# Kernel optimization log

Measured on AMD Instinct MI355X. Metric: run time of the kernel, lower is better.

The kernel has to match this reference:

```python
import jax, jax.numpy as jnp
import numpy as np

N_NODES = 100_000
N_EDGES = 800_000
D = 96
BN_EPS = 1e-5
LEAKY_SLOPE = 0.01


def setup_inputs() -> dict:
    key = jax.random.key(0)
    ks = jax.random.split(key, 9)
    x = jax.random.normal(ks[0], (N_NODES, D), dtype=jnp.float32)
    edge_index = jax.random.randint(ks[1], (2, N_EDGES), 0, N_NODES, dtype=jnp.int64)
    s = 0.05
    return {
        "x": x,
        "edge_index": edge_index,
        # SAGEConv #1 (mean aggregator, bias=False)
        "W_self1": jax.random.normal(ks[2], (D, D), dtype=jnp.float32) * s,
        "W_neigh1": jax.random.normal(ks[3], (D, D), dtype=jnp.float32) * s,
        # SAGEConv #2 (pool aggregator): fc_pool has bias, fc_self/fc_neigh bias=False
        "W_pool": jax.random.normal(ks[4], (D, D), dtype=jnp.float32) * s,
        "b_pool": jax.random.normal(ks[5], (D,), dtype=jnp.float32) * s,
        "W_self2": jax.random.normal(ks[6], (D, D), dtype=jnp.float32) * s,
        "W_neigh2": jax.random.normal(ks[7], (D, D), dtype=jnp.float32) * s,
        # BatchNorm affine params
        "g1": jnp.ones((D,), jnp.float32),
        "beta1": jnp.zeros((D,), jnp.float32),
        "g2": jnp.ones((D,), jnp.float32),
        "beta2": jnp.zeros((D,), jnp.float32),
    }


def _batch_norm(h, gamma, beta):
    # training-mode BatchNorm1d: biased batch stats over nodes
    mu = h.mean(axis=0)
    var = jnp.mean(jnp.square(h - mu), axis=0)
    return gamma * (h - mu) * jax.lax.rsqrt(var + BN_EPS) + beta


def _forward(x, edge_index, W_self1, W_neigh1, W_pool, b_pool, W_self2, W_neigh2,
             g1, beta1, g2, beta2):
    src, dst = edge_index[0], edge_index[1]
    n = x.shape[0]
    deg = jax.ops.segment_sum(jnp.ones((src.shape[0],), x.dtype), dst, num_segments=n)

    # ---- SAGEConv (mean): h_neigh = mean_{u in N(v)} x_u ; out = x W_self + h_neigh W_neigh
    agg_sum = jax.ops.segment_sum(x[src], dst, num_segments=n)          # [N, D]
    h_mean = agg_sum / jnp.maximum(deg, 1.0)[:, None]                   # 0 for isolated nodes
    out1 = x @ W_self1 + h_mean @ W_neigh1
    out1 = _batch_norm(out1, g1, beta1)

    # ---- SAGEConv (pool): h_neigh = max_{u in N(v)} relu(x_u W_pool + b_pool)
    hp = jax.nn.relu(x @ W_pool + b_pool)                               # [N, D]
    agg_max = jax.ops.segment_max(hp[src], dst, num_segments=n)        # -inf where empty
    h_max = jnp.where(deg[:, None] > 0, agg_max, 0.0)
    out2 = x @ W_self2 + h_max @ W_neigh2
    out2 = _batch_norm(out2, g2, beta2)

    return jax.nn.leaky_relu(out1 + out2, negative_slope=LEAKY_SLOPE)


def reference(x, edge_index, W_self1, W_neigh1, W_pool, b_pool, W_self2, W_neigh2,
              g1, beta1, g2, beta2):
    return _forward(x, edge_index, W_self1, W_neigh1, W_pool, b_pool,
                    W_self2, W_neigh2, g1, beta1, g2, beta2)
```

## Files before the change

### kernel.cpp

```cpp
#include <hip/hip_runtime.h>

#define NN 100000
#define NE 800000
#define DD 96
#define NROWPAD 100096
#define GBLK 782
#define SCAN_BLOCKS 100
#define SCAN_CHUNK 1000

typedef __attribute__((ext_vector_type(8))) short bf16x8;
typedef __attribute__((ext_vector_type(4))) float f32x4;
typedef unsigned short u16;
typedef unsigned int u32;

#define MFMA16 __builtin_amdgcn_mfma_f32_16x16x32_bf16

#define OFF_DEG      0u
#define OFF_ROWSTART 100000u
#define OFF_CURSOR   200004u
#define OFF_BSUM     300004u
#define OFF_STATS    300132u
#define OFF_PARAMS   300516u
#define OFF_WT       300900u
#define OFF_CSR      323940u
#define OFF_XH       1123940u
#define OFF_HMBF     10733156u
#define OFF_HXBF     15537764u

__device__ __forceinline__ u16 f2b(float f) {
  u32 u = __float_as_uint(f);
  u += 0x7FFFu + ((u >> 16) & 1u);
  return (u16)(u >> 16);
}
__device__ __forceinline__ float b2f(short h) {
  return __uint_as_float(((u32)(u16)h) << 16);
}

__global__ void wprep_kernel(const float* __restrict__ Ws1, const float* __restrict__ Wn1,
                             const float* __restrict__ Ws2, const float* __restrict__ Wn2,
                             const float* __restrict__ Wp, u16* __restrict__ wt) {
  int idx = blockIdx.x * 256 + threadIdx.x;
  if (idx >= 5 * 9216) return;
  int m = idx / 9216, r = idx % 9216;
  int k = r / 96, c = r % 96;
  const float* W = (m == 0) ? Ws1 : (m == 1) ? Wn1 : (m == 2) ? Ws2 : (m == 3) ? Wn2 : Wp;
  wt[m * 9216 + c * 96 + k] = f2b(W[k * 96 + c]);
}

__global__ void deg_kernel(const int* __restrict__ dst, int* __restrict__ deg) {
  int e = blockIdx.x * blockDim.x + threadIdx.x;
  if (e >= NE) return;
  atomicAdd(&deg[dst[e]], 1);
}

__global__ void scan_sum_kernel(const int* __restrict__ deg, int* __restrict__ bsum) {
  __shared__ int red[256];
  int t = threadIdx.x;
  int base = blockIdx.x * SCAN_CHUNK;
  int s = 0;
  for (int i = t; i < SCAN_CHUNK; i += 256) s += deg[base + i];
  red[t] = s;
  __syncthreads();
  for (int off = 128; off > 0; off >>= 1) {
    if (t < off) red[t] += red[t + off];
    __syncthreads();
  }
  if (t == 0) bsum[blockIdx.x] = red[0];
}

__global__ void scan_bsum_kernel(int* __restrict__ bsum, int* __restrict__ row_start) {
  __shared__ int sm[128];
  int t = threadIdx.x;
  int v = (t < SCAN_BLOCKS) ? bsum[t] : 0;
  sm[t] = v;
  __syncthreads();
  for (int off = 1; off < 128; off <<= 1) {
    int u = 0;
    if (t >= off) u = sm[t - off];
    __syncthreads();
    if (t >= off) sm[t] += u;
    __syncthreads();
  }
  if (t < SCAN_BLOCKS) bsum[t] = sm[t] - v;
  if (t == SCAN_BLOCKS - 1) row_start[NN] = sm[t];
}

__global__ void scan_final_kernel(const int* __restrict__ deg,
                                  const int* __restrict__ bsum,
                                  int* __restrict__ row_start,
                                  int* __restrict__ cursor) {
  __shared__ int sm[256];
  int t = threadIdx.x;
  int base = blockIdx.x * SCAN_CHUNK + t * 4;
  int4 d = {0, 0, 0, 0};
  if (t < 250) d = *reinterpret_cast<const int4*>(deg + base);
  int tot = d.x + d.y + d.z + d.w;
  sm[t] = tot;
  __syncthreads();
  for (int off = 1; off < 256; off <<= 1) {
    int u = 0;
    if (t >= off) u = sm[t - off];
    __syncthreads();
    if (t >= off) sm[t] += u;
    __syncthreads();
  }
  if (t < 250) {
    int run = bsum[blockIdx.x] + sm[t] - tot;
    int4 rs;
    rs.x = run;
    rs.y = run + d.x;
    rs.z = run + d.x + d.y;
    rs.w = run + d.x + d.y + d.z;
    *reinterpret_cast<int4*>(row_start + base) = rs;
    *reinterpret_cast<int4*>(cursor + base) = rs;
  }
}

__global__ void fill_csr_kernel(const int* __restrict__ src,
                                const int* __restrict__ dst,
                                int* __restrict__ cursor,
                                int* __restrict__ csr) {
  int e = blockIdx.x * blockDim.x + threadIdx.x;
  if (e >= NE) return;
  int pos = atomicAdd(&cursor[dst[e]], 1);
  csr[pos] = src[e];
}

__global__ __launch_bounds__(512) void hp_gemm_kernel(const float* __restrict__ x,
                                                      const u16* __restrict__ wt,
                                                      const float* __restrict__ bp,
                                                      u16* __restrict__ xh) {
  __shared__ bf16x8 wl[1152];
  int t = threadIdx.x;
  const bf16x8* wg = reinterpret_cast<const bf16x8*>(wt + 4 * 9216);
  for (int j = t; j < 1152; j += 512) wl[j] = wg[j];
  __syncthreads();
  int w = t >> 6, lane = t & 63;
  int i = lane & 15, g = lane >> 4;
  int row_base = blockIdx.x * 128 + w * 16;
  int grow_a = row_base + i;
  int lrow = grow_a < NN ? grow_a : NN - 1;
  const float4* xr = reinterpret_cast<const float4*>(x + (size_t)lrow * 96);
  bf16x8* xhv = reinterpret_cast<bf16x8*>(xh);
  bf16x8 ax[3];
#pragma unroll
  for (int kb = 0; kb < 3; ++kb) {
    float4 p = xr[(kb * 4 + g) * 2];
    float4 q = xr[(kb * 4 + g) * 2 + 1];
    bf16x8 v;
    v[0] = (short)f2b(p.x); v[1] = (short)f2b(p.y); v[2] = (short)f2b(p.z); v[3] = (short)f2b(p.w);
    v[4] = (short)f2b(q.x); v[5] = (short)f2b(q.y); v[6] = (short)f2b(q.z); v[7] = (short)f2b(q.w);
    ax[kb] = v;
    xhv[(size_t)grow_a * 24 + kb * 4 + g] = v;
  }
  for (int nt = 0; nt < 6; ++nt) {
    f32x4 acc = {0.f, 0.f, 0.f, 0.f};
    int bch = (nt * 16 + i) * 12;
#pragma unroll
    for (int kb = 0; kb < 3; ++kb)
      acc = MFMA16(ax[kb], wl[bch + kb * 4 + g], acc, 0, 0, 0);
    int col = nt * 16 + i;
    float bias = bp[col];
#pragma unroll
    for (int r = 0; r < 4; ++r) {
      int grow = row_base + g * 4 + r;
      xh[(size_t)grow * 192 + 96 + col] = f2b(fmaxf(acc[r] + bias, 0.0f));
    }
  }
}

__global__ __launch_bounds__(256) void gather_kernel(const u16* __restrict__ xh,
                                                     const int* __restrict__ row_start,
                                                     const int* __restrict__ csr,
                                                     u16* __restrict__ hmbf,
                                                     u16* __restrict__ hxbf) {
  int t = threadIdx.x;
  int node = blockIdx.x * 32 + (t & 31);
  int slot = t >> 5;
  bool isMax = slot >= 4;
  if (node >= NN) return;
  int beg = row_start[node], end = row_start[node + 1];
  int cbase = slot * 3;
  const bf16x8* XH = reinterpret_cast<const bf16x8*>(xh);
  float acc0[8], acc1[8], acc2[8];
#pragma unroll
  for (int j = 0; j < 8; ++j) { acc0[j] = 0.f; acc1[j] = 0.f; acc2[j] = 0.f; }
  int e = beg;
  for (; e + 2 <= end; e += 2) {
    size_t b0 = (size_t)csr[e] * 24 + cbase;
    size_t b1 = (size_t)csr[e + 1] * 24 + cbase;
    bf16x8 a0 = XH[b0], a1 = XH[b0 + 1], a2 = XH[b0 + 2];
    bf16x8 c0 = XH[b1], c1 = XH[b1 + 1], c2 = XH[b1 + 2];
    if (isMax) {
#pragma unroll
      for (int j = 0; j < 8; ++j) {
        acc0[j] = fmaxf(acc0[j], fmaxf(b2f(a0[j]), b2f(c0[j])));
        acc1[j] = fmaxf(acc1[j], fmaxf(b2f(a1[j]), b2f(c1[j])));
        acc2[j] = fmaxf(acc2[j], fmaxf(b2f(a2[j]), b2f(c2[j])));
      }
    } else {
#pragma unroll
      for (int j = 0; j < 8; ++j) {
        acc0[j] += b2f(a0[j]) + b2f(c0[j]);
        acc1[j] += b2f(a1[j]) + b2f(c1[j]);
        acc2[j] += b2f(a2[j]) + b2f(c2[j]);
      }
    }
  }
  if (e < end) {
    size_t b0 = (size_t)csr[e] * 24 + cbase;
    bf16x8 a0 = XH[b0], a1 = XH[b0 + 1], a2 = XH[b0 + 2];
    if (isMax) {
#pragma unroll
      for (int j = 0; j < 8; ++j) {
        acc0[j] = fmaxf(acc0[j], b2f(a0[j]));
        acc1[j] = fmaxf(acc1[j], b2f(a1[j]));
        acc2[j] = fmaxf(acc2[j], b2f(a2[j]));
      }
    } else {
#pragma unroll
      for (int j = 0; j < 8; ++j) {
        acc0[j] += b2f(a0[j]);
        acc1[j] += b2f(a1[j]);
        acc2[j] += b2f(a2[j]);
      }
    }
  }
  float scl = isMax ? 1.0f : ((end > beg) ? 1.0f / (float)(end - beg) : 0.0f);
  bf16x8 v0, v1, v2;
#pragma unroll
  for (int j = 0; j < 8; ++j) {
    v0[j] = (short)f2b(acc0[j] * scl);
    v1[j] = (short)f2b(acc1[j] * scl);
    v2[j] = (short)f2b(acc2[j] * scl);
  }
  u16* dstp = isMax ? hxbf : hmbf;
  int ccol = isMax ? (slot - 4) * 3 : slot * 3;
  size_t ob = (size_t)node * 12 + ccol;
  bf16x8* dv = reinterpret_cast<bf16x8*>(dstp);
  dv[ob] = v0; dv[ob + 1] = v1; dv[ob + 2] = v2;
}

__global__ __launch_bounds__(512) void dualgemm_kernel(const u16* __restrict__ xh,
                                                       const u16* __restrict__ hmbf,
                                                       const u16* __restrict__ hxbf,
                                                       const u16* __restrict__ wt,
                                                       float* __restrict__ stats,
                                                       const float* __restrict__ params,
                                                       float* __restrict__ out,
                                                       int mode) {
  __shared__ bf16x8 wl[4608];
  __shared__ float smst[384];
  int t = threadIdx.x;
  const bf16x8* wg = reinterpret_cast<const bf16x8*>(wt);
  for (int j = t; j < 4608; j += 512) wl[j] = wg[j];
  if (mode == 0)
    for (int j = t; j < 384; j += 512) smst[j] = 0.f;
  __syncthreads();
  int w = t >> 6, lane = t & 63;
  int i = lane & 15, g = lane >> 4;
  int row_base = blockIdx.x * 128 + w * 16;
  size_t arowx = (size_t)(row_base + i) * 24;
  size_t arowh = (size_t)(row_base + i) * 12;
  bf16x8 ax[3], am[3], ah[3];
#pragma unroll
  for (int kb = 0; kb < 3; ++kb) {
    ax[kb] = reinterpret_cast<const bf16x8*>(xh)[arowx + kb * 4 + g];
    am[kb] = reinterpret_cast<const bf16x8*>(hmbf)[arowh + kb * 4 + g];
    ah[kb] = reinterpret_cast<const bf16x8*>(hxbf)[arowh + kb * 4 + g];
  }
  for (int nt = 0; nt < 6; ++nt) {
    f32x4 a1 = {0.f, 0.f, 0.f, 0.f}, a2 = {0.f, 0.f, 0.f, 0.f};
    int bch = (nt * 16 + i) * 12;
#pragma unroll
    for (int kb = 0; kb < 3; ++kb) {
      int bc = bch + kb * 4 + g;
      a1 = MFMA16(ax[kb], wl[bc], a1, 0, 0, 0);
      a1 = MFMA16(am[kb], wl[1152 + bc], a1, 0, 0, 0);
      a2 = MFMA16(ax[kb], wl[2304 + bc], a2, 0, 0, 0);
      a2 = MFMA16(ah[kb], wl[3456 + bc], a2, 0, 0, 0);
    }
    int col = nt * 16 + i;
    if (mode == 0) {
      float s1 = 0, q1 = 0, s2 = 0, q2 = 0;
#pragma unroll
      for (int r = 0; r < 4; ++r) {
        int grow = row_base + g * 4 + r;
        if (grow < NN) {
          float v = a1[r], u = a2[r];
          s1 += v; q1 += v * v; s2 += u; q2 += u * u;
        }
      }
      s1 += __shfl_xor(s1, 16); q1 += __shfl_xor(q1, 16);
      s2 += __shfl_xor(s2, 16); q2 += __shfl_xor(q2, 16);
      s1 += __shfl_xor(s1, 32); q1 += __shfl_xor(q1, 32);
      s2 += __shfl_xor(s2, 32); q2 += __shfl_xor(q2, 32);
      if (g == 0) {
        atomicAdd(&smst[col], s1);
        atomicAdd(&smst[96 + col], q1);
        atomicAdd(&smst[192 + col], s2);
        atomicAdd(&smst[288 + col], q2);
      }
    } else {
      float p1 = params[col], c1 = params[96 + col];
      float p2 = params[192 + col], c2 = params[288 + col];
#pragma unroll
      for (int r = 0; r < 4; ++r) {
        int grow = row_base + g * 4 + r;
        if (grow < NN) {
          float v = p1 * a1[r] + c1 + p2 * a2[r] + c2;
          v = v > 0.f ? v : 0.01f * v;
          out[(size_t)grow * 96 + col] = v;
        }
      }
    }
  }
  if (mode == 0) {
    __syncthreads();
    for (int j = t; j < 384; j += 512) atomicAdd(&stats[j], smst[j]);
  }
}

__global__ void finalize_kernel(const float* __restrict__ stats,
                                const float* __restrict__ g1, const float* __restrict__ beta1,
                                const float* __restrict__ g2, const float* __restrict__ beta2,
                                float* __restrict__ params) {
  int c = threadIdx.x;
  if (c >= 96) return;
  const float inv_n = 1.0f / NN;
  float mu1 = stats[c] * inv_n;
  float var1 = fmaxf(stats[96 + c] * inv_n - mu1 * mu1, 0.0f);
  float is1 = rsqrtf(var1 + 1e-5f);
  float a1 = g1[c] * is1;
  params[c] = a1;
  params[96 + c] = beta1[c] - a1 * mu1;
  float mu2 = stats[192 + c] * inv_n;
  float var2 = fmaxf(stats[288 + c] * inv_n - mu2 * mu2, 0.0f);
  float is2 = rsqrtf(var2 + 1e-5f);
  float a2 = g2[c] * is2;
  params[192 + c] = a2;
  params[288 + c] = beta2[c] - a2 * mu2;
}

extern "C" void kernel_launch(void* const* d_in, const int* in_sizes, int n_in,
                              void* d_out, int out_size, void* d_ws, size_t ws_size,
                              hipStream_t stream) {
  const float* x       = (const float*)d_in[0];
  const int*   ei      = (const int*)d_in[1];
  const float* W_self1 = (const float*)d_in[2];
  const float* W_neigh1= (const float*)d_in[3];
  const float* W_pool  = (const float*)d_in[4];
  const float* b_pool  = (const float*)d_in[5];
  const float* W_self2 = (const float*)d_in[6];
  const float* W_neigh2= (const float*)d_in[7];
  const float* g1      = (const float*)d_in[8];
  const float* beta1   = (const float*)d_in[9];
  const float* g2      = (const float*)d_in[10];
  const float* beta2   = (const float*)d_in[11];
  float* out = (float*)d_out;

  float* ws = (float*)d_ws;
  int*   deg       = (int*)(ws + OFF_DEG);
  int*   row_start = (int*)(ws + OFF_ROWSTART);
  int*   cursor    = (int*)(ws + OFF_CURSOR);
  int*   bsum      = (int*)(ws + OFF_BSUM);
  float* stats     = ws + OFF_STATS;
  float* params    = ws + OFF_PARAMS;
  u16*   wt        = (u16*)(ws + OFF_WT);
  int*   csr       = (int*)(ws + OFF_CSR);
  u16*   xh        = (u16*)(ws + OFF_XH);
  u16*   hmbf      = (u16*)(ws + OFF_HMBF);
  u16*   hxbf      = (u16*)(ws + OFF_HXBF);

  const int* src = ei;
  const int* dst = ei + NE;

  hipMemsetAsync(deg, 0, NN * sizeof(int), stream);
  hipMemsetAsync(stats, 0, 384 * sizeof(float), stream);

  wprep_kernel<<<(5 * 9216 + 255) / 256, 256, 0, stream>>>(W_self1, W_neigh1, W_self2,
                                                           W_neigh2, W_pool, wt);

  deg_kernel<<<(NE + 255) / 256, 256, 0, stream>>>(dst, deg);
  scan_sum_kernel<<<SCAN_BLOCKS, 256, 0, stream>>>(deg, bsum);
  scan_bsum_kernel<<<1, 128, 0, stream>>>(bsum, row_start);
  scan_final_kernel<<<SCAN_BLOCKS, 256, 0, stream>>>(deg, bsum, row_start, cursor);
  fill_csr_kernel<<<(NE + 255) / 256, 256, 0, stream>>>(src, dst, cursor, csr);

  hp_gemm_kernel<<<GBLK, 512, 0, stream>>>(x, wt, b_pool, xh);

  gather_kernel<<<(NN + 31) / 32, 256, 0, stream>>>(xh, row_start, csr, hmbf, hxbf);

  dualgemm_kernel<<<GBLK, 512, 0, stream>>>(xh, hmbf, hxbf, wt, stats, params, out, 0);
  finalize_kernel<<<1, 128, 0, stream>>>(stats, g1, beta1, g2, beta2, params);
  dualgemm_kernel<<<GBLK, 512, 0, stream>>>(xh, hmbf, hxbf, wt, stats, params, out, 1);
}
```

Baseline: 278.0 us.

## Store pre-BN GEMM outputs and apply BN with an elementwise pass; retile gather

The dual GEMM now runs once. It writes its bf16 pre-normalization outputs in place over the aggregated-feature buffers while it accumulates the BN statistics, so the second full GEMM pass that recomputed the same products is gone. A new vectorized elementwise kernel applies the BN affine transform and leaky ReLU from those stored values. The gather kernel is also retiled to 12 slots of 16 columns per node with 4-edge unrolling, to get more memory-level parallelism. In exchange, the intermediate outputs are rounded to bf16 before normalization, and the GEMM uses 1024-thread blocks with an extra barrier to make the in-place overwrite safe.

Result: no change. 274.2 us (-1.4%).

```diff
diff --git a/kernel.cpp b/kernel.cpp
--- a/kernel.cpp
+++ b/kernel.cpp
@@ -5,6 +5,7 @@
 #define DD 96
 #define NROWPAD 100096
 #define GBLK 782
+#define DBLK 391
 #define SCAN_BLOCKS 100
 #define SCAN_CHUNK 1000
 
@@ -169,7 +170,7 @@
   }
 }
 
-__global__ __launch_bounds__(256) void gather_kernel(const u16* __restrict__ xh,
+__global__ __launch_bounds__(384) void gather_kernel(const u16* __restrict__ xh,
                                                      const int* __restrict__ row_start,
                                                      const int* __restrict__ csr,
                                                      u16* __restrict__ hmbf,
@@ -177,89 +178,84 @@
   int t = threadIdx.x;
   int node = blockIdx.x * 32 + (t & 31);
   int slot = t >> 5;
-  bool isMax = slot >= 4;
+  bool isMax = slot >= 6;
   if (node >= NN) return;
   int beg = row_start[node], end = row_start[node + 1];
-  int cbase = slot * 3;
+  int cbase = slot * 2;
   const bf16x8* XH = reinterpret_cast<const bf16x8*>(xh);
-  float acc0[8], acc1[8], acc2[8];
-#pragma unroll
-  for (int j = 0; j < 8; ++j) { acc0[j] = 0.f; acc1[j] = 0.f; acc2[j] = 0.f; }
+  float a0[8], a1[8];
+#pragma unroll
+  for (int j = 0; j < 8; ++j) { a0[j] = 0.f; a1[j] = 0.f; }
   int e = beg;
-  for (; e + 2 <= end; e += 2) {
+  for (; e + 4 <= end; e += 4) {
     size_t b0 = (size_t)csr[e] * 24 + cbase;
     size_t b1 = (size_t)csr[e + 1] * 24 + cbase;
-    bf16x8 a0 = XH[b0], a1 = XH[b0 + 1], a2 = XH[b0 + 2];
-    bf16x8 c0 = XH[b1], c1 = XH[b1 + 1], c2 = XH[b1 + 2];
+    size_t b2 = (size_t)csr[e + 2] * 24 + cbase;
+    size_t b3 = (size_t)csr[e + 3] * 24 + cbase;
+    bf16x8 u0 = XH[b0], v0 = XH[b0 + 1];
+    bf16x8 u1 = XH[b1], v1 = XH[b1 + 1];
+    bf16x8 u2 = XH[b2], v2 = XH[b2 + 1];
+    bf16x8 u3 = XH[b3], v3 = XH[b3 + 1];
     if (isMax) {
 #pragma unroll
       for (int j = 0; j < 8; ++j) {
-        acc0[j] = fmaxf(acc0[j], fmaxf(b2f(a0[j]), b2f(c0[j])));
-        acc1[j] = fmaxf(acc1[j], fmaxf(b2f(a1[j]), b2f(c1[j])));
-        acc2[j] = fmaxf(acc2[j], fmaxf(b2f(a2[j]), b2f(c2[j])));
+        a0[j] = fmaxf(a0[j], fmaxf(fmaxf(b2f(u0[j]), b2f(u1[j])), fmaxf(b2f(u2[j]), b2f(u3[j]))));
+        a1[j] = fmaxf(a1[j], fmaxf(fmaxf(b2f(v0[j]), b2f(v1[j])), fmaxf(b2f(v2[j]), b2f(v3[j]))));
       }
     } else {
 #pragma unroll
       for (int j = 0; j < 8; ++j) {
-        acc0[j] += b2f(a0[j]) + b2f(c0[j]);
-        acc1[j] += b2f(a1[j]) + b2f(c1[j]);
-        acc2[j] += b2f(a2[j]) + b2f(c2[j]);
+        a0[j] += (b2f(u0[j]) + b2f(u1[j])) + (b2f(u2[j]) + b2f(u3[j]));
+        a1[j] += (b2f(v0[j]) + b2f(v1[j])) + (b2f(v2[j]) + b2f(v3[j]));
       }
     }
   }
-  if (e < end) {
+  for (; e < end; ++e) {
     size_t b0 = (size_t)csr[e] * 24 + cbase;
-    bf16x8 a0 = XH[b0], a1 = XH[b0 + 1], a2 = XH[b0 + 2];
+    bf16x8 u0 = XH[b0], v0 = XH[b0 + 1];
     if (isMax) {
 #pragma unroll
       for (int j = 0; j < 8; ++j) {
-        acc0[j] = fmaxf(acc0[j], b2f(a0[j]));
-        acc1[j] = fmaxf(acc1[j], b2f(a1[j]));
-        acc2[j] = fmaxf(acc2[j], b2f(a2[j]));
+        a0[j] = fmaxf(a0[j], b2f(u0[j]));
+        a1[j] = fmaxf(a1[j], b2f(v0[j]));
       }
     } else {
 #pragma unroll
       for (int j = 0; j < 8; ++j) {
-        acc0[j] += b2f(a0[j]);
-        acc1[j] += b2f(a1[j]);
-        acc2[j] += b2f(a2[j]);
+        a0[j] += b2f(u0[j]);
+        a1[j] += b2f(v0[j]);
       }
     }
   }
   float scl = isMax ? 1.0f : ((end > beg) ? 1.0f / (float)(end - beg) : 0.0f);
-  bf16x8 v0, v1, v2;
+  bf16x8 w0, w1;
 #pragma unroll
   for (int j = 0; j < 8; ++j) {
-    v0[j] = (short)f2b(acc0[j] * scl);
-    v1[j] = (short)f2b(acc1[j] * scl);
-    v2[j] = (short)f2b(acc2[j] * scl);
+    w0[j] = (short)f2b(a0[j] * scl);
+    w1[j] = (short)f2b(a1[j] * scl);
   }
   u16* dstp = isMax ? hxbf : hmbf;
-  int ccol = isMax ? (slot - 4) * 3 : slot * 3;
-  size_t ob = (size_t)node * 12 + ccol;
+  int outc = isMax ? (slot - 6) * 2 : slot * 2;
   bf16x8* dv = reinterpret_cast<bf16x8*>(dstp);
-  dv[ob] = v0; dv[ob + 1] = v1; dv[ob + 2] = v2;
-}
-
-__global__ __launch_bounds__(512) void dualgemm_kernel(const u16* __restrict__ xh,
-                                                       const u16* __restrict__ hmbf,
-                                                       const u16* __restrict__ hxbf,
-                                                       const u16* __restrict__ wt,
-                                                       float* __restrict__ stats,
-                                                       const float* __restrict__ params,
-                                                       float* __restrict__ out,
-                                                       int mode) {
+  size_t ob = (size_t)node * 12 + outc;
+  dv[ob] = w0; dv[ob + 1] = w1;
+}
+
+__global__ __launch_bounds__(1024) void dualgemm_kernel(const u16* __restrict__ xh,
+                                                        u16* __restrict__ hmbf,
+                                                        u16* __restrict__ hxbf,
+                                                        const u16* __restrict__ wt,
+                                                        float* __restrict__ stats) {
   __shared__ bf16x8 wl[4608];
   __shared__ float smst[384];
   int t = threadIdx.x;
   const bf16x8* wg = reinterpret_cast<const bf16x8*>(wt);
-  for (int j = t; j < 4608; j += 512) wl[j] = wg[j];
-  if (mode == 0)
-    for (int j = t; j < 384; j += 512) smst[j] = 0.f;
+  for (int j = t; j < 4608; j += 1024) wl[j] = wg[j];
+  for (int j = t; j < 384; j += 1024) smst[j] = 0.f;
   __syncthreads();
   int w = t >> 6, lane = t & 63;
   int i = lane & 15, g = lane >> 4;
-  int row_base = blockIdx.x * 128 + w * 16;
+  int row_base = blockIdx.x * 256 + w * 16;
   size_t arowx = (size_t)(row_base + i) * 24;
   size_t arowh = (size_t)(row_base + i) * 12;
   bf16x8 ax[3], am[3], ah[3];
@@ -269,6 +265,7 @@
     am[kb] = reinterpret_cast<const bf16x8*>(hmbf)[arowh + kb * 4 + g];
     ah[kb] = reinterpret_cast<const bf16x8*>(hxbf)[arowh + kb * 4 + g];
   }
+  __syncthreads();
   for (int nt = 0; nt < 6; ++nt) {
     f32x4 a1 = {0.f, 0.f, 0.f, 0.f}, a2 = {0.f, 0.f, 0.f, 0.f};
     int bch = (nt * 16 + i) * 12;
@@ -281,44 +278,30 @@
       a2 = MFMA16(ah[kb], wl[3456 + bc], a2, 0, 0, 0);
     }
     int col = nt * 16 + i;
-    if (mode == 0) {
-      float s1 = 0, q1 = 0, s2 = 0, q2 = 0;
-#pragma unroll
-      for (int r = 0; r < 4; ++r) {
-        int grow = row_base + g * 4 + r;
-        if (grow < NN) {
-          float v = a1[r], u = a2[r];
-          s1 += v; q1 += v * v; s2 += u; q2 += u * u;
-        }
+    float s1 = 0, q1 = 0, s2 = 0, q2 = 0;
+#pragma unroll
+    for (int r = 0; r < 4; ++r) {
+      int grow = row_base + g * 4 + r;
+      if (grow < NN) {
+        float v = a1[r], u = a2[r];
+        s1 += v; q1 += v * v; s2 += u; q2 += u * u;
+        hmbf[(size_t)grow * 96 + col] = f2b(v);
+        hxbf[(size_t)grow * 96 + col] = f2b(u);
       }
-      s1 += __shfl_xor(s1, 16); q1 += __shfl_xor(q1, 16);
-      s2 += __shfl_xor(s2, 16); q2 += __shfl_xor(q2, 16);
-      s1 += __shfl_xor(s1, 32); q1 += __shfl_xor(q1, 32);
-      s2 += __shfl_xor(s2, 32); q2 += __shfl_xor(q2, 32);
-      if (g == 0) {
-        atomicAdd(&smst[col], s1);
-        atomicAdd(&smst[96 + col], q1);
-        atomicAdd(&smst[192 + col], s2);
-        atomicAdd(&smst[288 + col], q2);
-      }
-    } else {
-      float p1 = params[col], c1 = params[96 + col];
-      float p2 = params[192 + col], c2 = params[288 + col];
-#pragma unroll
-      for (int r = 0; r < 4; ++r) {
-        int grow = row_base + g * 4 + r;
-        if (grow < NN) {
-          float v = p1 * a1[r] + c1 + p2 * a2[r] + c2;
-          v = v > 0.f ? v : 0.01f * v;
-          out[(size_t)grow * 96 + col] = v;
-        }
-      }
-    }
-  }
-  if (mode == 0) {
-    __syncthreads();
-    for (int j = t; j < 384; j += 512) atomicAdd(&stats[j], smst[j]);
-  }
+    }
+    s1 += __shfl_xor(s1, 16); q1 += __shfl_xor(q1, 16);
+    s2 += __shfl_xor(s2, 16); q2 += __shfl_xor(q2, 16);
+    s1 += __shfl_xor(s1, 32); q1 += __shfl_xor(q1, 32);
+    s2 += __shfl_xor(s2, 32); q2 += __shfl_xor(q2, 32);
+    if (g == 0) {
+      atomicAdd(&smst[col], s1);
+      atomicAdd(&smst[96 + col], q1);
+      atomicAdd(&smst[192 + col], s2);
+      atomicAdd(&smst[288 + col], q2);
+    }
+  }
+  __syncthreads();
+  for (int j = t; j < 384; j += 1024) atomicAdd(&stats[j], smst[j]);
 }
 
 __global__ void finalize_kernel(const float* __restrict__ stats,
@@ -342,6 +325,36 @@
   params[288 + c] = beta2[c] - a2 * mu2;
 }
 
+__global__ __launch_bounds__(256) void final_kernel(const u16* __restrict__ o1,
+                                                    const u16* __restrict__ o2,
+                                                    const float* __restrict__ params,
+                                                    float* __restrict__ out) {
+  int idx = blockIdx.x * 256 + threadIdx.x;
+  if (idx >= NN * 12) return;
+  int c8 = idx % 12;
+  bf16x8 v1 = reinterpret_cast<const bf16x8*>(o1)[idx];
+  bf16x8 v2 = reinterpret_cast<const bf16x8*>(o2)[idx];
+  const float4* P = reinterpret_cast<const float4*>(params);
+  float4 A1l = P[c8 * 2],      A1h = P[c8 * 2 + 1];
+  float4 B1l = P[24 + c8 * 2], B1h = P[24 + c8 * 2 + 1];
+  float4 A2l = P[48 + c8 * 2], A2h = P[48 + c8 * 2 + 1];
+  float4 B2l = P[72 + c8 * 2], B2h = P[72 + c8 * 2 + 1];
+  float A1[8] = {A1l.x, A1l.y, A1l.z, A1l.w, A1h.x, A1h.y, A1h.z, A1h.w};
+  float B1[8] = {B1l.x, B1l.y, B1l.z, B1l.w, B1h.x, B1h.y, B1h.z, B1h.w};
+  float A2[8] = {A2l.x, A2l.y, A2l.z, A2l.w, A2h.x, A2h.y, A2h.z, A2h.w};
+  float B2[8] = {B2l.x, B2l.y, B2l.z, B2l.w, B2h.x, B2h.y, B2h.z, B2h.w};
+  float o[8];
+#pragma unroll
+  for (int j = 0; j < 8; ++j) {
+    float v = A1[j] * b2f(v1[j]) + B1[j] + A2[j] * b2f(v2[j]) + B2[j];
+    o[j] = v > 0.f ? v : 0.01f * v;
+  }
+  float4* ov = reinterpret_cast<float4*>(out);
+  float4 lo = {o[0], o[1], o[2], o[3]}, hi = {o[4], o[5], o[6], o[7]};
+  ov[idx * 2] = lo;
+  ov[idx * 2 + 1] = hi;
+}
+
 extern "C" void kernel_launch(void* const* d_in, const int* in_sizes, int n_in,
                               void* d_out, int out_size, void* d_ws, size_t ws_size,
                               hipStream_t stream) {
@@ -389,9 +402,9 @@
 
   hp_gemm_kernel<<<GBLK, 512, 0, stream>>>(x, wt, b_pool, xh);
 
-  gather_kernel<<<(NN + 31) / 32, 256, 0, stream>>>(xh, row_start, csr, hmbf, hxbf);
-
-  dualgemm_kernel<<<GBLK, 512, 0, stream>>>(xh, hmbf, hxbf, wt, stats, params, out, 0);
+  gather_kernel<<<(NN + 31) / 32, 384, 0, stream>>>(xh, row_start, csr, hmbf, hxbf);
+
+  dualgemm_kernel<<<DBLK, 1024, 0, stream>>>(xh, hmbf, hxbf, wt, stats);
   finalize_kernel<<<1, 128, 0, stream>>>(stats, g1, beta1, g2, beta2, params);
-  dualgemm_kernel<<<GBLK, 512, 0, stream>>>(xh, hmbf, hxbf, wt, stats, params, out, 1);
-}
+  final_kernel<<<(NN * 12 + 255) / 256, 256, 0, stream>>>(hmbf, hxbf, params, out);
+}
```
